# Kernel tuning notes

Measured on AMD Instinct MI355X. Metric: run time of the kernel, lower is better.

The kernel has to match this reference:

```python
import jax, jax.numpy as jnp
import numpy as np

T = 1.0  # temperature from __init__ (t=1)


def setup_inputs() -> dict:
    key = jax.random.key(0)
    k1, k2, k3 = jax.random.split(key, 3)
    N, C, D = 262144, 1024, 128
    feats = jax.random.normal(k1, (N, D), dtype=jnp.float32)
    prototypes = jax.random.normal(k2, (C, D), dtype=jnp.float32)
    labels = jax.random.randint(k3, (N,), 0, C, dtype=jnp.int64)
    return {"feats": feats, "prototypes": prototypes, "labels": labels}


def _dce_loss(feats, prototypes, labels):
    # same math as sqrt(sum((x[:,None,:]-y)**2, -1)) without the NxCxD tensor.
    x_sq = jnp.sum(feats * feats, axis=-1, keepdims=True)          # [N,1]
    y_sq = jnp.sum(prototypes * prototypes, axis=-1)               # [C]
    xy = jnp.einsum('nd,cd->nc', feats, prototypes)                # [N,C]
    sq_dist = jnp.maximum(x_sq + y_sq[None, :] - 2.0 * xy, 0.0)
    logits = -jnp.sqrt(sq_dist) / T                                # [N,C]
    logp = jax.nn.log_softmax(logits, axis=-1)
    nll = -jnp.take_along_axis(logp, labels[:, None], axis=-1)[:, 0]
    return jnp.mean(nll)  # CrossEntropyLoss default reduction='mean'


def reference(feats, prototypes, labels):
    return _dce_loss(feats, prototypes, labels)
```

## Files before the change

### kernel.cpp

```cpp
#include <hip/hip_runtime.h>
#include <hip/hip_bf16.h>

typedef __bf16 bf16x8 __attribute__((ext_vector_type(8)));
typedef __bf16 bf16x2 __attribute__((ext_vector_type(2)));
typedef float f32x4 __attribute__((ext_vector_type(4)));

#define LN2f 0.6931471805599453f
#define CEf  2.0402785445f

__global__ void dce_prep(const float* __restrict__ protos,
                         unsigned short* __restrict__ bpf,
                         float* __restrict__ ysqn) {
    int c = blockIdx.x;
    int lane = threadIdx.x;
    float2 f = ((const float2*)(protos))[c * 64 + lane];
    int d0 = lane * 2;
    int kk = d0 >> 5, sub = d0 & 31, lg = sub >> 3, e = sub & 7;
    size_t o = (((size_t)((c >> 4) * 4 + kk) * 64) + lg * 16 + (c & 15)) * 8 + e;
    bf16x2 h;
    h.x = (__bf16)f.x;
    h.y = (__bf16)f.y;
    *(bf16x2*)(bpf + o) = h;
    float xs = f.x * f.x + f.y * f.y;
#pragma unroll
    for (int d = 1; d < 64; d <<= 1) xs += __shfl_xor(xs, d);
    if (lane == 0) ysqn[c] = -0.5f * xs;
}

__global__ __launch_bounds__(256, 4) void dce_main(
    const float* __restrict__ feats,
    const float* __restrict__ protos,
    const unsigned short* __restrict__ bpf,
    const float* __restrict__ ysqn,
    const int* __restrict__ labels,
    float* __restrict__ partials, int C) {
    const int tid = threadIdx.x;
    const int lane = tid & 63;
    const int w = tid >> 6;
    const int row0 = blockIdx.x * 128;
    const int rbase = row0 + w * 32;
    const int lr = lane & 15;
    const int lg = lane >> 4;

    const int r1 = row0 + (tid >> 1);
    const int half = tid & 1;
    const int lab = labels[r1];
    const float4* fx = (const float4*)feats + (size_t)r1 * 32 + half * 16;
    const float4* px = (const float4*)protos + (size_t)lab * 32 + half * 16;
    float xx = 0.f, yy = 0.f, xy = 0.f;
#pragma unroll
    for (int i = 0; i < 16; ++i) {
        float4 f = fx[i], p = px[i];
        xx = fmaf(f.x, f.x, fmaf(f.y, f.y, fmaf(f.z, f.z, fmaf(f.w, f.w, xx))));
        yy = fmaf(p.x, p.x, fmaf(p.y, p.y, fmaf(p.z, p.z, fmaf(p.w, p.w, yy))));
        xy = fmaf(f.x, p.x, fmaf(f.y, p.y, fmaf(f.z, p.z, fmaf(f.w, p.w, xy))));
    }
    xx += __shfl_xor(xx, 1);
    yy += __shfl_xor(yy, 1);
    xy += __shfl_xor(xy, 1);
    const float ld = __builtin_amdgcn_sqrtf(fmaxf(fmaf(-2.f, xy, xx + yy), 0.f));

    bf16x8 a[2][4];
    const float4* f4 = (const float4*)feats;
#pragma unroll
    for (int m = 0; m < 2; ++m) {
        size_t r = (size_t)(rbase + m * 16 + lr);
#pragma unroll
        for (int kk = 0; kk < 4; ++kk) {
            size_t idx = r * 32 + kk * 8 + lg * 2;
            float4 lo = f4[idx];
            float4 hi = f4[idx + 1];
            bf16x8 v;
            v[0] = (__bf16)lo.x; v[1] = (__bf16)lo.y; v[2] = (__bf16)lo.z; v[3] = (__bf16)lo.w;
            v[4] = (__bf16)hi.x; v[5] = (__bf16)hi.y; v[6] = (__bf16)hi.z; v[7] = (__bf16)hi.w;
            a[m][kk] = v;
        }
    }

    float pre[2][4];
#pragma unroll
    for (int m = 0; m < 2; ++m)
#pragma unroll
        for (int reg = 0; reg < 4; ++reg)
            pre[m][reg] = -0.5f * __shfl(xx, 2 * (m * 16 + lg * 4 + reg));

    float lacc[2][4];
#pragma unroll
    for (int m = 0; m < 2; ++m)
#pragma unroll
        for (int reg = 0; reg < 4; ++reg) lacc[m][reg] = 0.f;

    const char* bp = (const char*)bpf + (size_t)lane * 16;
    const float* ysp = ysqn + lr;

    const int t0 = ((w << 4) + ((blockIdx.x & 15) << 2)) & 63;

#define LOADB(dst, yq, t)                                                     \
    {                                                                         \
        const int tt_ = (t0 + (t)) & 63;                                      \
        _Pragma("unroll") for (int kk = 0; kk < 4; ++kk)                      \
            dst[kk] = *(const bf16x8*)(bp + (size_t)tt_ * 4096 + kk * 1024);  \
        yq = ysp[tt_ * 16];                                                   \
    }

#define COMPUTE(b, yq)                                                          \
    {                                                                           \
        _Pragma("unroll") for (int m = 0; m < 2; ++m) {                         \
            f32x4 acc;                                                          \
            acc[0] = pre[m][0] + yq;                                            \
            acc[1] = pre[m][1] + yq;                                            \
            acc[2] = pre[m][2] + yq;                                            \
            acc[3] = pre[m][3] + yq;                                            \
            acc = __builtin_amdgcn_mfma_f32_16x16x32_bf16(a[m][0], b[0], acc, 0, 0, 0); \
            acc = __builtin_amdgcn_mfma_f32_16x16x32_bf16(a[m][1], b[1], acc, 0, 0, 0); \
            acc = __builtin_amdgcn_mfma_f32_16x16x32_bf16(a[m][2], b[2], acc, 0, 0, 0); \
            acc = __builtin_amdgcn_mfma_f32_16x16x32_bf16(a[m][3], b[3], acc, 0, 0, 0); \
            _Pragma("unroll") for (int reg = 0; reg < 4; ++reg) {               \
                float s = __builtin_amdgcn_sqrtf(-acc[reg]);   \
                lacc[m][reg] += __builtin_amdgcn_exp2f(s * -CEf);               \
            }                                                                   \
        }                                                                       \
    }

    bf16x8 bA[4], bB[4];
    float yqA, yqB;
    LOADB(bA, yqA, 0);
    const int nt = C >> 4;
    for (int t = 0; t < nt - 2; t += 2) {
        LOADB(bB, yqB, t + 1);
        COMPUTE(bA, yqA);
        LOADB(bA, yqA, t + 2);
        COMPUTE(bB, yqB);
    }
    LOADB(bB, yqB, nt - 1);
    COMPUTE(bA, yqA);
    COMPUTE(bB, yqB);

#undef LOADB
#undef COMPUTE

    float ssum = 0.f;
#pragma unroll
    for (int m = 0; m < 2; ++m)
#pragma unroll
        for (int reg = 0; reg < 4; ++reg) {
            float l = lacc[m][reg];
            l += __shfl_xor(l, 1);
            l += __shfl_xor(l, 2);
            l += __shfl_xor(l, 4);
            l += __shfl_xor(l, 8);
            float ldv = __shfl(ld, 2 * (m * 16 + lg * 4 + reg));
            if (lr == 0) ssum += ldv + LN2f * __builtin_amdgcn_logf(l);
        }
    ssum += __shfl_xor(ssum, 16);
    ssum += __shfl_xor(ssum, 32);

    __shared__ float red[4];
    if (lane == 0) red[w] = ssum;
    __syncthreads();
    if (tid == 0) partials[blockIdx.x] = red[0] + red[1] + red[2] + red[3];
}

__global__ void dce_finish(const float* __restrict__ partials,
                           float* __restrict__ out, int nblocks, float invN) {
    int tid = threadIdx.x;
    float s = 0.f;
    for (int i = tid; i < nblocks; i += 256) s += partials[i];
#pragma unroll
    for (int d = 1; d < 64; d <<= 1) s += __shfl_xor(s, d);
    __shared__ float red[4];
    if ((tid & 63) == 0) red[tid >> 6] = s;
    __syncthreads();
    if (tid == 0) out[0] = (red[0] + red[1] + red[2] + red[3]) * invN;
}

extern "C" void kernel_launch(void* const* d_in, const int* in_sizes, int n_in,
                              void* d_out, int out_size, void* d_ws, size_t ws_size,
                              hipStream_t stream) {
    const float* feats = (const float*)d_in[0];
    const float* protos = (const float*)d_in[1];
    const int* labels = (const int*)d_in[2];
    const int N = in_sizes[2];
    const int C = in_sizes[1] / 128;
    float* out = (float*)d_out;

    unsigned short* bpf = (unsigned short*)d_ws;
    float* ysqn = (float*)((char*)d_ws + (size_t)C * 128 * 2);
    float* partials = ysqn + C;
    const int nblocks = N / 128;

    dce_prep<<<C, 64, 0, stream>>>(protos, bpf, ysqn);
    dce_main<<<nblocks, 256, 0, stream>>>(feats, protos, bpf, ysqn, labels, partials, C);
    dce_finish<<<1, 256, 0, stream>>>(partials, out, nblocks, 1.0f / (float)N);
}
```

Before: 138.8 us.

## Stage prototype B tiles through double-buffered LDS with direct global-to-LDS loads

Each wave used to read the bf16 prototype tiles directly from global memory into registers. Now the block cooperatively copies 16 KB chunks into two LDS buffers with global_load_lds, prefetching the next chunk while computing on the current one. All four waves read B from LDS. This cuts global/L2 traffic roughly fourfold per block but adds a barrier per chunk and 32 KB of LDS per block, which may limit occupancy under launch_bounds(256,4).

```diff
diff --git a/kernel.cpp b/kernel.cpp
--- a/kernel.cpp
+++ b/kernel.cpp
@@ -7,6 +7,13 @@
 
 #define LN2f 0.6931471805599453f
 #define CEf  2.0402785445f
+
+typedef __attribute__((address_space(3))) unsigned int lds_u32;
+typedef __attribute__((address_space(1))) unsigned int glb_u32;
+
+__device__ __forceinline__ void gload16(const void* g, void* l) {
+    __builtin_amdgcn_global_load_lds((const glb_u32*)g, (lds_u32*)l, 16, 0, 0);
+}
 
 __global__ void dce_prep(const float* __restrict__ protos,
                          unsigned short* __restrict__ bpf,
@@ -42,6 +49,22 @@
     const int lr = lane & 15;
     const int lg = lane >> 4;
 
+    __shared__ __align__(16) unsigned char bsm0[16384];
+    __shared__ __align__(16) unsigned char bsm1[16384];
+    __shared__ float red[4];
+
+    const char* bpc = (const char*)bpf;
+    const int c0 = (blockIdx.x >> 3) & 15;
+
+#define STAGE(buf, chunkIdx)                                                   \
+    {                                                                          \
+        const char* src_ = bpc + (size_t)(chunkIdx) * 16384 + tid * 16;        \
+        _Pragma("unroll") for (int kt = 0; kt < 4; ++kt)                       \
+            gload16(src_ + kt * 4096, (buf) + kt * 4096 + tid * 16);           \
+    }
+
+    STAGE(bsm0, c0);
+
     const int r1 = row0 + (tid >> 1);
     const int half = tid & 1;
     const int lab = labels[r1];
@@ -90,54 +113,50 @@
 #pragma unroll
         for (int reg = 0; reg < 4; ++reg) lacc[m][reg] = 0.f;
 
-    const char* bp = (const char*)bpf + (size_t)lane * 16;
     const float* ysp = ysqn + lr;
 
-    const int t0 = ((w << 4) + ((blockIdx.x & 15) << 2)) & 63;
-
-#define LOADB(dst, yq, t)                                                     \
-    {                                                                         \
-        const int tt_ = (t0 + (t)) & 63;                                      \
-        _Pragma("unroll") for (int kk = 0; kk < 4; ++kk)                      \
-            dst[kk] = *(const bf16x8*)(bp + (size_t)tt_ * 4096 + kk * 1024);  \
-        yq = ysp[tt_ * 16];                                                   \
-    }
-
-#define COMPUTE(b, yq)                                                          \
+#define TILE(buf, kt, tt)                                                       \
     {                                                                           \
+        const bf16x8* bl_ = (const bf16x8*)((buf) + (kt) * 4096);               \
+        bf16x8 b0 = bl_[lane];                                                  \
+        bf16x8 b1 = bl_[64 + lane];                                             \
+        bf16x8 b2 = bl_[128 + lane];                                            \
+        bf16x8 b3 = bl_[192 + lane];                                            \
+        const float yq_ = ysp[(tt) * 16];                                       \
         _Pragma("unroll") for (int m = 0; m < 2; ++m) {                         \
             f32x4 acc;                                                          \
-            acc[0] = pre[m][0] + yq;                                            \
-            acc[1] = pre[m][1] + yq;                                            \
-            acc[2] = pre[m][2] + yq;                                            \
-            acc[3] = pre[m][3] + yq;                                            \
-            acc = __builtin_amdgcn_mfma_f32_16x16x32_bf16(a[m][0], b[0], acc, 0, 0, 0); \
-            acc = __builtin_amdgcn_mfma_f32_16x16x32_bf16(a[m][1], b[1], acc, 0, 0, 0); \
-            acc = __builtin_amdgcn_mfma_f32_16x16x32_bf16(a[m][2], b[2], acc, 0, 0, 0); \
-            acc = __builtin_amdgcn_mfma_f32_16x16x32_bf16(a[m][3], b[3], acc, 0, 0, 0); \
+            acc[0] = pre[m][0] + yq_;                                           \
+            acc[1] = pre[m][1] + yq_;                                           \
+            acc[2] = pre[m][2] + yq_;                                           \
+            acc[3] = pre[m][3] + yq_;                                           \
+            acc = __builtin_amdgcn_mfma_f32_16x16x32_bf16(a[m][0], b0, acc, 0, 0, 0); \
+            acc = __builtin_amdgcn_mfma_f32_16x16x32_bf16(a[m][1], b1, acc, 0, 0, 0); \
+            acc = __builtin_amdgcn_mfma_f32_16x16x32_bf16(a[m][2], b2, acc, 0, 0, 0); \
+            acc = __builtin_amdgcn_mfma_f32_16x16x32_bf16(a[m][3], b3, acc, 0, 0, 0); \
             _Pragma("unroll") for (int reg = 0; reg < 4; ++reg) {               \
-                float s = __builtin_amdgcn_sqrtf(-acc[reg]);   \
-                lacc[m][reg] += __builtin_amdgcn_exp2f(s * -CEf);               \
+                float s_ = __builtin_amdgcn_sqrtf(-acc[reg]);                   \
+                lacc[m][reg] += __builtin_amdgcn_exp2f(s_ * -CEf);              \
             }                                                                   \
         }                                                                       \
     }
 
-    bf16x8 bA[4], bB[4];
-    float yqA, yqB;
-    LOADB(bA, yqA, 0);
-    const int nt = C >> 4;
-    for (int t = 0; t < nt - 2; t += 2) {
-        LOADB(bB, yqB, t + 1);
-        COMPUTE(bA, yqA);
-        LOADB(bA, yqA, t + 2);
-        COMPUTE(bB, yqB);
-    }
-    LOADB(bB, yqB, nt - 1);
-    COMPUTE(bA, yqA);
-    COMPUTE(bB, yqB);
-
-#undef LOADB
-#undef COMPUTE
+    __syncthreads();
+#pragma unroll 2
+    for (int ch = 0; ch < 16; ++ch) {
+        unsigned char* curb = (ch & 1) ? bsm1 : bsm0;
+        unsigned char* nxtb = (ch & 1) ? bsm0 : bsm1;
+        const int ci = (c0 + ch) & 15;
+        if (ch + 1 < 16) {
+            const int ni = (c0 + ch + 1) & 15;
+            STAGE(nxtb, ni);
+        }
+#pragma unroll
+        for (int kt = 0; kt < 4; ++kt) TILE(curb, kt, ci * 4 + kt);
+        __syncthreads();
+    }
+
+#undef STAGE
+#undef TILE
 
     float ssum = 0.f;
 #pragma unroll
@@ -155,7 +174,6 @@
     ssum += __shfl_xor(ssum, 16);
     ssum += __shfl_xor(ssum, 32);
 
-    __shared__ float red[4];
     if (lane == 0) red[w] = ssum;
     __syncthreads();
     if (tid == 0) partials[blockIdx.x] = red[0] + red[1] + red[2] + red[3];
```

Measured after the change: 127.2 us. 8.3% less time.
